# Optimization experiments

Measured on AMD Instinct MI355X. Metric: run time of the kernel, lower is better.

The kernel has to match this reference:

```python
import jax, jax.numpy as jnp
import numpy as np

NUM_CODES = 1024
CODE_DIM = 256
EMA_DECAY = 0.99
COMMITMENT = 0.25
EPS = 1e-6


def setup_inputs() -> dict:
    key = jax.random.key(0)
    k1, k2 = jax.random.split(key)
    z = jax.random.normal(k1, (64, 512, CODE_DIM), dtype=jnp.float32)
    embedding = jax.random.normal(k2, (NUM_CODES, CODE_DIM), dtype=jnp.float32)
    cluster_size = jnp.zeros((NUM_CODES,), dtype=jnp.float32)
    embedding_avg = embedding.copy()
    return {"z": z, "embedding": embedding, "cluster_size": cluster_size,
            "embedding_avg": embedding_avg}


def reference(z, embedding, cluster_size, embedding_avg):
    K, D = embedding.shape
    flat = z.reshape(-1, D)                                  # [N, D]
    dist = (jnp.sum(flat * flat, axis=1, keepdims=True)
            - 2.0 * (flat @ embedding.T)
            + jnp.sum(embedding * embedding, axis=1))
    indices = jnp.argmin(dist, axis=1)                       # [N]
    z_q = embedding[indices].reshape(z.shape)

    # EMA codebook update (training branch, no-grad in original)
    counts = jax.ops.segment_sum(jnp.ones_like(indices, dtype=flat.dtype),
                                 indices, num_segments=K)    # one-hot col sums
    embed_sum = jax.ops.segment_sum(flat, indices, num_segments=K)  # [K, D]
    new_cluster_size = cluster_size * EMA_DECAY + (1.0 - EMA_DECAY) * counts
    new_embedding_avg = embedding_avg * EMA_DECAY + (1.0 - EMA_DECAY) * embed_sum
    n = jnp.sum(new_cluster_size)
    cs = (new_cluster_size + EPS) / (n + K * EPS)
    new_embedding = new_embedding_avg / cs[:, None]

    loss = COMMITMENT * jnp.mean((jax.lax.stop_gradient(z_q) - z) ** 2)
    z_q_st = z + jax.lax.stop_gradient(z_q - z)
    return (z_q_st, loss, indices, new_cluster_size, new_embedding_avg,
            new_embedding)
```

## Files before the change

kernel.cpp:

```cpp
#include <hip/hip_runtime.h>

#define N_ROWS   32768
#define KCODES   1024
#define DDIM     256
#define RPB      64
#define NBLK     512

#define O_ZQ     0
#define O_LOSS   8388608
#define O_IDX    8388609
#define O_NCS    8421377
#define O_NEA    8422401
#define O_NEMB   8684545

#define W_ESUM   0
#define W_CNT    262144
#define W_ENORM  263168
#define W_LOSSP  264192
#define W_N      265728
#define W_IDX    265792
#define W_SORT   298560
#define W_RANK   331328

typedef _Float16 half_t;
typedef __attribute__((ext_vector_type(8))) _Float16 half8;
typedef __attribute__((ext_vector_type(4))) float floatx4;

__global__ __launch_bounds__(256)
void k_prep2(const float* __restrict__ emb, float* __restrict__ enorm,
             half_t* __restrict__ Bp, float* __restrict__ zero_ws) {
    __shared__ half_t hi[16 * 256];
    __shared__ half_t lo[16 * 256];
    __shared__ float  ssum[256];
    const int ct  = blockIdx.x;
    const int tid = threadIdx.x;
    const int c16 = tid >> 4;
    const int dp  = tid & 15;

    {
        float4 z4 = {0.f, 0.f, 0.f, 0.f};
        float4* wsf4 = (float4*)zero_ws;
        int t = ct * 256 + tid;
        #pragma unroll
        for (int i = 0; i < 4; ++i) wsf4[t + i * 16384] = z4;
        if (t < 256) wsf4[65536 + t] = z4;
    }

    float ss = 0.f;
    #pragma unroll
    for (int i = 0; i < 4; ++i) {
        float4 v = *(const float4*)(emb + (size_t)(ct * 16 + c16) * DDIM + dp * 16 + i * 4);
        ss += v.x * v.x + v.y * v.y + v.z * v.z + v.w * v.w;
        #pragma unroll
        for (int q = 0; q < 4; ++q) {
            float f = (&v.x)[q];
            half_t h = (half_t)f;
            hi[c16 * 256 + dp * 16 + i * 4 + q] = h;
            lo[c16 * 256 + dp * 16 + i * 4 + q] = (half_t)(f - (float)h);
        }
    }
    ssum[tid] = ss;
    __syncthreads();
    if (tid < 16) {
        float s = 0.f;
        #pragma unroll
        for (int i = 0; i < 16; ++i) s += ssum[tid * 16 + i];
        enorm[ct * 16 + tid] = s;
    }

    const int g16 = ((ct >> 4) << 2) | ((ct >> 2) & 3);
    const int ns  = ct & 3;
    #pragma unroll
    for (int i = 0; i < 4; ++i) {
        int f    = tid + i * 256;
        int ks   = f >> 6;
        int lane = f & 63;
        int cc   = lane & 15;
        int seg  = ks >> 3;
        int ko   = (ks & 7) * 32 + (lane >> 4) * 8;
        const half_t* src = (seg == 1) ? lo : hi;
        half8 v = *(const half8*)(src + cc * 256 + ko);
        *(half8*)(Bp + (((size_t)(g16 * 16 + ks) * 4 + ns) * 64 + lane) * 8) = v;
    }
}

__global__ __launch_bounds__(512)
void k_argmin(const float* __restrict__ z, const half_t* __restrict__ Bp,
              const float* __restrict__ enorm, const float* __restrict__ embf,
              int* __restrict__ out_idx, float* __restrict__ out_idx_f,
              float* __restrict__ out_zq, float* __restrict__ lossp,
              int* __restrict__ counts_i, int* __restrict__ rank_ws) {
    __shared__ __align__(16) half_t As[RPB * 512];

    const int tid  = threadIdx.x;
    const int w    = tid >> 6;
    const int lane = tid & 63;
    const int tx   = lane & 15;
    const int quad = lane >> 4;
    const int rh   = w >> 2;
    const int cq   = w & 3;
    const int rbase = blockIdx.x * RPB;

    {
        const int arow = w * 8 + (lane >> 3);
        const int sw   = arow & 7;
        #pragma unroll
        for (int it = 0; it < 4; ++it) {
            int g = it * 8 + (lane & 7);
            const float* zp = z + (size_t)(rbase + arow) * DDIM + g * 8;
            float4 v0 = *(const float4*)zp;
            float4 v1 = *(const float4*)(zp + 4);
            half8 hi, lo;
            hi[0] = (half_t)v0.x; lo[0] = (half_t)(v0.x - (float)hi[0]);
            hi[1] = (half_t)v0.y; lo[1] = (half_t)(v0.y - (float)hi[1]);
            hi[2] = (half_t)v0.z; lo[2] = (half_t)(v0.z - (float)hi[2]);
            hi[3] = (half_t)v0.w; lo[3] = (half_t)(v0.w - (float)hi[3]);
            hi[4] = (half_t)v1.x; lo[4] = (half_t)(v1.x - (float)hi[4]);
            hi[5] = (half_t)v1.y; lo[5] = (half_t)(v1.y - (float)hi[5]);
            hi[6] = (half_t)v1.z; lo[6] = (half_t)(v1.z - (float)hi[6]);
            hi[7] = (half_t)v1.w; lo[7] = (half_t)(v1.w - (float)hi[7]);
            *(half8*)(&As[arow * 512 + ((g ^ sw)) * 8])        = hi;
            *(half8*)(&As[arow * 512 + (((32 + g) ^ sw)) * 8]) = lo;
        }
    }
    __syncthreads();

    floatx4 zero4 = {0.f, 0.f, 0.f, 0.f};
    float bd[2][4];
    int   bi[2][4];
    #pragma unroll
    for (int mt = 0; mt < 2; ++mt)
        #pragma unroll
        for (int r = 0; r < 4; ++r) { bd[mt][r] = 3.402823466e38f; bi[mt][r] = 0; }

    for (int g4 = 0; g4 < 4; ++g4) {
        const int cb = cq * 256 + g4 * 64;
        const half_t* Bg = Bp + (size_t)(cq * 4 + g4) * 32768 + (size_t)lane * 8;

        floatx4 acc[2][4];
        #pragma unroll
        for (int mt = 0; mt < 2; ++mt)
            #pragma unroll
            for (int ns = 0; ns < 4; ++ns) acc[mt][ns] = zero4;

        half8 B0[4], B1[4];
        #define LOADB(PK, BUF)                                                 \
            { const half_t* bp_ = Bg + (PK) * 2048;                            \
              _Pragma("unroll")                                                \
              for (int ns = 0; ns < 4; ++ns)                                   \
                  BUF[ns] = *(const half8*)(bp_ + ns * 512); }
        #define MFMA_BLK(AF, BUF)                                              \
            _Pragma("unroll")                                                  \
            for (int mt = 0; mt < 2; ++mt)                                     \
                _Pragma("unroll")                                              \
                for (int ns = 0; ns < 4; ++ns)                                 \
                    acc[mt][ns] = __builtin_amdgcn_mfma_f32_16x16x32_f16(      \
                        AF[mt], BUF[ns], acc[mt][ns], 0, 0, 0);

        LOADB(0, B0);
        LOADB(1, B1);

        #pragma unroll 2
        for (int s = 0; s < 8; ++s) {
            half8 a0[2], a1[2];
            #pragma unroll
            for (int mt = 0; mt < 2; ++mt) {
                int row = rh * 32 + mt * 16 + tx;
                int sw  = row & 7;
                a0[mt] = *(half8*)(&As[row * 512 + ((s * 4 + quad) ^ sw) * 8]);
                a1[mt] = *(half8*)(&As[row * 512 + ((32 + s * 4 + quad) ^ sw) * 8]);
            }
            if (s & 1) { MFMA_BLK(a0, B1) MFMA_BLK(a1, B1) LOADB(s + 2, B1); }
            else       { MFMA_BLK(a0, B0) MFMA_BLK(a1, B0) LOADB(s + 2, B0); }
        }
        #pragma unroll 2
        for (int s = 8; s < 16; ++s) {
            half8 a0[2];
            #pragma unroll
            for (int mt = 0; mt < 2; ++mt) {
                int row = rh * 32 + mt * 16 + tx;
                int sw  = row & 7;
                a0[mt] = *(half8*)(&As[row * 512 + (((s - 8) * 4 + quad) ^ sw) * 8]);
            }
            if (s & 1) { MFMA_BLK(a0, B1) if (s + 2 < 16) LOADB(s + 2, B1); }
            else       { MFMA_BLK(a0, B0) if (s + 2 < 16) LOADB(s + 2, B0); }
        }
        #undef LOADB
        #undef MFMA_BLK

        #pragma unroll
        for (int ns = 0; ns < 4; ++ns) {
            float en = enorm[cb + ns * 16 + tx];
            int   cc = cb + ns * 16 + tx;
            #pragma unroll
            for (int mt = 0; mt < 2; ++mt)
                #pragma unroll
                for (int r = 0; r < 4; ++r) {
                    float d = fmaf(-2.f, acc[mt][ns][r], en);
                    if (d < bd[mt][r]) { bd[mt][r] = d; bi[mt][r] = cc; }
                }
        }
    }

    #pragma unroll
    for (int mt = 0; mt < 2; ++mt)
        #pragma unroll
        for (int r = 0; r < 4; ++r) {
            float d = bd[mt][r];
            int   b = bi[mt][r];
            #pragma unroll
            for (int off = 8; off > 0; off >>= 1) {
                float od = __shfl_xor(d, off);
                int   ob = __shfl_xor(b, off);
                if (od < d || (od == d && ob < b)) { d = od; b = ob; }
            }
            bd[mt][r] = d; bi[mt][r] = b;
        }

    __syncthreads();
    float* sd   = (float*)As;
    int*   si   = ((int*)As) + 256;
    int*   sidx = ((int*)As) + 512;
    if (tx == 0) {
        #pragma unroll
        for (int mt = 0; mt < 2; ++mt)
            #pragma unroll
            for (int r = 0; r < 4; ++r) {
                int row = rh * 32 + mt * 16 + quad * 4 + r;
                sd[row * 4 + cq] = bd[mt][r];
                si[row * 4 + cq] = bi[mt][r];
            }
    }
    __syncthreads();
    if (tid < RPB) {
        int row = tid;
        float d = sd[row * 4];
        int   b = si[row * 4];
        #pragma unroll
        for (int ww = 1; ww < 4; ++ww) {
            float od = sd[row * 4 + ww];
            int   ob = si[row * 4 + ww];
            if (od < d || (od == d && ob < b)) { d = od; b = ob; }
        }
        sidx[row] = b;
        out_idx[rbase + row]   = b;
        out_idx_f[rbase + row] = (float)b;
        int rk = atomicAdd(&counts_i[b], 1);
        rank_ws[rbase + row] = rk;
    }
    __syncthreads();

    float l = 0.f;
    #pragma unroll
    for (int u = 0; u < 8; ++u) {
        int gi  = tid + u * 512;
        int row = gi >> 6;
        int c4  = gi & 63;
        int k   = sidx[row];
        float4 zv = *(const float4*)(z    + (size_t)(rbase + row) * DDIM + c4 * 4);
        float4 ev = *(const float4*)(embf + (size_t)k * DDIM + c4 * 4);
        float dx = ev.x - zv.x, dy = ev.y - zv.y, dz = ev.z - zv.z, dw = ev.w - zv.w;
        float4 o = { zv.x + dx, zv.y + dy, zv.z + dz, zv.w + dw };
        *(float4*)(out_zq + (size_t)(rbase + row) * DDIM + c4 * 4) = o;
        l += dx * dx + dy * dy + dz * dz + dw * dw;
    }
    #pragma unroll
    for (int off = 32; off > 0; off >>= 1) l += __shfl_down(l, off);
    __shared__ float ls[8];
    if (lane == 0) ls[w] = l;
    __syncthreads();
    if (tid == 0) {
        float s = 0.f;
        #pragma unroll
        for (int i = 0; i < 8; ++i) s += ls[i];
        lossp[blockIdx.x] = s;
    }
}

__global__ __launch_bounds__(256)
void k_scatter(const float* __restrict__ cs_in, const int* __restrict__ counts_i,
               const float* __restrict__ lossp, const int* __restrict__ idx,
               const int* __restrict__ rank_ws, int* __restrict__ rows_sorted,
               float* __restrict__ out_ncs, float* __restrict__ n_ws,
               float* __restrict__ loss_out) {
    const int tid = threadIdx.x;
    const int bid = blockIdx.x;
    __shared__ int ps[256];
    __shared__ int base_s[1024];
    __shared__ float sv[4], sl[4];

    int c[4]; int pt = 0;
    #pragma unroll
    for (int i = 0; i < 4; ++i) { c[i] = counts_i[tid * 4 + i]; pt += c[i]; }
    ps[tid] = pt;
    __syncthreads();
    for (int s = 1; s < 256; s <<= 1) {
        int v = (tid >= s) ? ps[tid - s] : 0;
        __syncthreads();
        ps[tid] += v;
        __syncthreads();
    }
    int o = ps[tid] - pt;
    float v = 0.f;
    #pragma unroll
    for (int i = 0; i < 4; ++i) {
        base_s[tid * 4 + i] = o;
        o += c[i];
        if (bid == 0) {
            float nc = cs_in[tid * 4 + i] * 0.99f + 0.01f * (float)c[i];
            out_ncs[tid * 4 + i] = nc;
            v += nc;
        }
    }
    if (bid == 0) {
        float l = lossp[tid] + lossp[tid + 256];
        #pragma unroll
        for (int off = 32; off > 0; off >>= 1) {
            v += __shfl_down(v, off);
            l += __shfl_down(l, off);
        }
        if ((tid & 63) == 0) { sv[tid >> 6] = v; sl[tid >> 6] = l; }
    }
    __syncthreads();
    if (bid == 0 && tid == 0) {
        n_ws[0]     = sv[0] + sv[1] + sv[2] + sv[3];
        loss_out[0] = 0.25f * ((sl[0] + sl[1] + sl[2] + sl[3]) / 8388608.0f);
    }
    int r = bid * 256 + tid;
    int k = idx[r];
    rows_sorted[base_s[k] + rank_ws[r]] = r;
}

__global__ __launch_bounds__(256)
void k_esum2(const float* __restrict__ z, const int* __restrict__ rows_sorted,
             const int* __restrict__ idx, float* __restrict__ esum) {
    const int tid  = threadIdx.x;
    const int w    = tid >> 6;
    const int lane = tid & 63;
    const int base = (blockIdx.x * 4 + w) * 32;

    int r = rows_sorted[base + (lane & 31)];
    int c = idx[r];
    float4 acc = {0.f, 0.f, 0.f, 0.f};
    #pragma unroll 8
    for (int j = 0; j < 32; ++j) {
        int rj = __shfl(r, j);
        int cj = __shfl(c, j);
        float4 zv = *(const float4*)(z + (size_t)rj * DDIM + lane * 4);
        acc.x += zv.x; acc.y += zv.y; acc.z += zv.z; acc.w += zv.w;
        int cn = (j < 31) ? __shfl(c, j + 1) : -1;
        if (cn != cj) {
            float* p = esum + (size_t)cj * DDIM + lane * 4;
            atomicAdd(p + 0, acc.x);
            atomicAdd(p + 1, acc.y);
            atomicAdd(p + 2, acc.z);
            atomicAdd(p + 3, acc.w);
            acc.x = 0.f; acc.y = 0.f; acc.z = 0.f; acc.w = 0.f;
        }
    }
}

__global__ __launch_bounds__(256)
void k_embed(const float* __restrict__ ea, const float* __restrict__ esum,
             const float* __restrict__ ncs, const float* __restrict__ n_ws,
             float* __restrict__ out_nea, float* __restrict__ out_nemb) {
    const int tid = threadIdx.x;
    const int kb  = blockIdx.x * 4;
    const int c   = tid >> 6;
    const int l   = tid & 63;
    size_t off = (size_t)(kb + c) * DDIM + l * 4;
    float4 av = *(const float4*)(ea   + off);
    float4 ev = *(const float4*)(esum + off);
    float4 nea = { av.x * 0.99f + 0.01f * ev.x,
                   av.y * 0.99f + 0.01f * ev.y,
                   av.z * 0.99f + 0.01f * ev.z,
                   av.w * 0.99f + 0.01f * ev.w };
    *(float4*)(out_nea + off) = nea;
    float csv = (ncs[kb + c] + 1e-6f) / (n_ws[0] + 0.001024f);
    float4 nemb = { nea.x / csv, nea.y / csv, nea.z / csv, nea.w / csv };
    *(float4*)(out_nemb + off) = nemb;
}

extern "C" void kernel_launch(void* const* d_in, const int* in_sizes, int n_in,
                              void* d_out, int out_size, void* d_ws, size_t ws_size,
                              hipStream_t stream) {
    const float* z   = (const float*)d_in[0];
    const float* emb = (const float*)d_in[1];
    const float* cs  = (const float*)d_in[2];
    const float* ea  = (const float*)d_in[3];
    float* out = (float*)d_out;
    float* ws  = (float*)d_ws;

    float* esum    = ws + W_ESUM;
    int*   cnts    = (int*)(ws + W_CNT);
    float* enorm   = ws + W_ENORM;
    float* lossp   = ws + W_LOSSP;
    float* wn      = ws + W_N;
    int*   widx    = (int*)(ws + W_IDX);
    int*   rsorted = (int*)(ws + W_SORT);
    int*   rankw   = (int*)(ws + W_RANK);

    half_t* Bp = (half_t*)(out + O_NEA + 3);

    k_prep2   <<<64, 256, 0, stream>>>(emb, enorm, Bp, ws);
    k_argmin  <<<NBLK, 512, 0, stream>>>(z, Bp, enorm, emb,
                                         widx, out + O_IDX, out + O_ZQ, lossp,
                                         cnts, rankw);
    k_scatter <<<128, 256, 0, stream>>>(cs, cnts, lossp, widx, rankw, rsorted,
                                        out + O_NCS, wn, out + O_LOSS);
    k_esum2   <<<256, 256, 0, stream>>>(z, rsorted, widx, esum);
    k_embed   <<<256, 256, 0, stream>>>(ea, esum, out + O_NCS, wn,
                                        out + O_NEA, out + O_NEMB);
}
```

Baseline: 179.8 us.

## Fuse scatter and segment-sum kernels, building sorted row lists in shared memory

Merges the counting-sort scatter kernel and the embed-sum kernel into one. Each block redoes the prefix scan over counts, then scans all 32768 indices and ranks to collect in shared memory just the 128 sorted rows it owns, and finally accumulates z rows into esum with atomics. This removes one kernel launch and the global rows_sorted round trip. In exchange every block re-reads the full idx and rank arrays (256 blocks × 256 KB), which adds redundant global/L2 traffic.

```diff
diff --git a/kernel.cpp b/kernel.cpp
--- a/kernel.cpp
+++ b/kernel.cpp
@@ -19,7 +19,6 @@
 #define W_LOSSP  264192
 #define W_N      265728
 #define W_IDX    265792
-#define W_SORT   298560
 #define W_RANK   331328
 
 typedef _Float16 half_t;
@@ -278,15 +277,19 @@
 }
 
 __global__ __launch_bounds__(256)
-void k_scatter(const float* __restrict__ cs_in, const int* __restrict__ counts_i,
-               const float* __restrict__ lossp, const int* __restrict__ idx,
-               const int* __restrict__ rank_ws, int* __restrict__ rows_sorted,
-               float* __restrict__ out_ncs, float* __restrict__ n_ws,
-               float* __restrict__ loss_out) {
+void k_esum4(const float* __restrict__ z, const int* __restrict__ idx,
+             const int* __restrict__ rank_ws, const int* __restrict__ counts_i,
+             const float* __restrict__ cs_in, const float* __restrict__ lossp,
+             float* __restrict__ esum, float* __restrict__ out_ncs,
+             float* __restrict__ n_ws, float* __restrict__ loss_out) {
     const int tid = threadIdx.x;
     const int bid = blockIdx.x;
+    const int w    = tid >> 6;
+    const int lane = tid & 63;
+    const int p0  = bid * 128;
     __shared__ int ps[256];
     __shared__ int base_s[1024];
+    __shared__ int list[128];
     __shared__ float sv[4], sl[4];
 
     int c[4]; int pt = 0;
@@ -326,36 +329,44 @@
         n_ws[0]     = sv[0] + sv[1] + sv[2] + sv[3];
         loss_out[0] = 0.25f * ((sl[0] + sl[1] + sl[2] + sl[3]) / 8388608.0f);
     }
-    int r = bid * 256 + tid;
-    int k = idx[r];
-    rows_sorted[base_s[k] + rank_ws[r]] = r;
-}
-
-__global__ __launch_bounds__(256)
-void k_esum2(const float* __restrict__ z, const int* __restrict__ rows_sorted,
-             const int* __restrict__ idx, float* __restrict__ esum) {
-    const int tid  = threadIdx.x;
-    const int w    = tid >> 6;
-    const int lane = tid & 63;
-    const int base = (blockIdx.x * 4 + w) * 32;
-
-    int r = rows_sorted[base + (lane & 31)];
-    int c = idx[r];
-    float4 acc = {0.f, 0.f, 0.f, 0.f};
-    #pragma unroll 8
-    for (int j = 0; j < 32; ++j) {
-        int rj = __shfl(r, j);
-        int cj = __shfl(c, j);
-        float4 zv = *(const float4*)(z + (size_t)rj * DDIM + lane * 4);
-        acc.x += zv.x; acc.y += zv.y; acc.z += zv.z; acc.w += zv.w;
-        int cn = (j < 31) ? __shfl(c, j + 1) : -1;
-        if (cn != cj) {
-            float* p = esum + (size_t)cj * DDIM + lane * 4;
-            atomicAdd(p + 0, acc.x);
-            atomicAdd(p + 1, acc.y);
-            atomicAdd(p + 2, acc.z);
-            atomicAdd(p + 3, acc.w);
-            acc.x = 0.f; acc.y = 0.f; acc.z = 0.f; acc.w = 0.f;
+
+    {
+        const int4* ip = (const int4*)idx;
+        const int4* rp = (const int4*)rank_ws;
+        #pragma unroll 4
+        for (int it = 0; it < 32; ++it) {
+            int e  = tid + it * 256;
+            int4 kv = ip[e];
+            int4 rv = rp[e];
+            int r0 = e * 4;
+            int pos;
+            pos = base_s[kv.x] + rv.x; if ((unsigned)(pos - p0) < 128u) list[pos - p0] = r0;
+            pos = base_s[kv.y] + rv.y; if ((unsigned)(pos - p0) < 128u) list[pos - p0] = r0 + 1;
+            pos = base_s[kv.z] + rv.z; if ((unsigned)(pos - p0) < 128u) list[pos - p0] = r0 + 2;
+            pos = base_s[kv.w] + rv.w; if ((unsigned)(pos - p0) < 128u) list[pos - p0] = r0 + 3;
+        }
+    }
+    __syncthreads();
+
+    {
+        int r = list[w * 32 + (lane & 31)];
+        int cc = idx[r];
+        float4 acc = {0.f, 0.f, 0.f, 0.f};
+        #pragma unroll 8
+        for (int j = 0; j < 32; ++j) {
+            int rj = __shfl(r, j);
+            int cj = __shfl(cc, j);
+            float4 zv = *(const float4*)(z + (size_t)rj * DDIM + lane * 4);
+            acc.x += zv.x; acc.y += zv.y; acc.z += zv.z; acc.w += zv.w;
+            int cn = (j < 31) ? __shfl(cc, j + 1) : -1;
+            if (cn != cj) {
+                float* p = esum + (size_t)cj * DDIM + lane * 4;
+                atomicAdd(p + 0, acc.x);
+                atomicAdd(p + 1, acc.y);
+                atomicAdd(p + 2, acc.z);
+                atomicAdd(p + 3, acc.w);
+                acc.x = 0.f; acc.y = 0.f; acc.z = 0.f; acc.w = 0.f;
+            }
         }
     }
 }
@@ -397,18 +408,16 @@
     float* lossp   = ws + W_LOSSP;
     float* wn      = ws + W_N;
     int*   widx    = (int*)(ws + W_IDX);
-    int*   rsorted = (int*)(ws + W_SORT);
     int*   rankw   = (int*)(ws + W_RANK);
 
     half_t* Bp = (half_t*)(out + O_NEA + 3);
 
-    k_prep2   <<<64, 256, 0, stream>>>(emb, enorm, Bp, ws);
-    k_argmin  <<<NBLK, 512, 0, stream>>>(z, Bp, enorm, emb,
-                                         widx, out + O_IDX, out + O_ZQ, lossp,
-                                         cnts, rankw);
-    k_scatter <<<128, 256, 0, stream>>>(cs, cnts, lossp, widx, rankw, rsorted,
-                                        out + O_NCS, wn, out + O_LOSS);
-    k_esum2   <<<256, 256, 0, stream>>>(z, rsorted, widx, esum);
-    k_embed   <<<256, 256, 0, stream>>>(ea, esum, out + O_NCS, wn,
-                                        out + O_NEA, out + O_NEMB);
+    k_prep2  <<<64, 256, 0, stream>>>(emb, enorm, Bp, ws);
+    k_argmin <<<NBLK, 512, 0, stream>>>(z, Bp, enorm, emb,
+                                        widx, out + O_IDX, out + O_ZQ, lossp,
+                                        cnts, rankw);
+    k_esum4  <<<256, 256, 0, stream>>>(z, widx, rankw, cnts, cs, lossp,
+                                       esum, out + O_NCS, wn, out + O_LOSS);
+    k_embed  <<<256, 256, 0, stream>>>(ea, esum, out + O_NCS, wn,
+                                       out + O_NEA, out + O_NEMB);
 }
```

Measured after the change: 194.4 us. 8.1% more time.
